# Performance work log

Measured on AMD Instinct MI355X. Metric: run time of the kernel, lower is better.

## Reference

```python
import jax, jax.numpy as jnp
import numpy as np

B, W, F = 32, 128, 64      # batch, window (node feat dim), n_features (nodes)
H, D = 2, 128              # num_heads, out_window_size
NEG_SLOPE = 0.2


def setup_inputs() -> dict:
    key = jax.random.key(0)
    k1, k2, k3, k4, k5 = jax.random.split(key, 5)
    s = 1.0 / np.sqrt(W)
    return {
        "x": jax.random.normal(k1, (B, W, F), dtype=jnp.float32),
        "Wl": jax.random.normal(k2, (W, H * D), dtype=jnp.float32) * s,   # fc_src
        "Wr": jax.random.normal(k3, (W, H * D), dtype=jnp.float32) * s,   # fc_dst
        "attn_a": jax.random.normal(k4, (H, D), dtype=jnp.float32) * s,   # GATv2 attn vector
        "bias": jax.random.normal(k5, (H * D,), dtype=jnp.float32) * 0.01,
    }


def reference(x, Wl, Wr, attn_a, bias):
    """Dense batched GATv2 over a complete graph (with self loops) per batch.

    Matches DGL GATv2Conv (share_weights=False, bias=True, eval mode so
    feat_drop/attn_drop are identity), followed by mean over heads and the
    [B,F,D] -> [B,D,F] transpose of DGLFeatureGAT.forward.
    """
    # node features: x [B, W, F] -> [B, F, W]
    xn = jnp.swapaxes(x, 1, 2)
    el = jnp.einsum('bnw,whd->bnhd', xn, Wl.reshape(W, H, D))  # fc_src(h)
    er = jnp.einsum('bnw,whd->bnhd', xn, Wr.reshape(W, H, D))  # fc_dst(h)
    # edge (src=j -> dst=i): e_ij = a_h . LeakyReLU(el_j + er_i)
    pair = el[:, None, :, :, :] + er[:, :, None, :, :]          # [B, i, j, H, D]
    e = jnp.einsum('bijhd,hd->bhij', jax.nn.leaky_relu(pair, NEG_SLOPE), attn_a)
    # softmax over incoming edges (src j) per dst i
    alpha = jax.nn.softmax(e, axis=-1)                          # [B, H, i, j]
    rst = jnp.einsum('bhij,bjhd->bihd', alpha, el)              # aggregate fc_src feats
    rst = rst + bias.reshape(1, 1, H, D)
    out = rst.mean(axis=2)                                      # mean over heads -> [B, F, D]
    return jnp.swapaxes(out, 1, 2)                              # [B, D, F]
```

## Files before the change

### kernel.cpp

```cpp
#include <hip/hip_runtime.h>
#include <hip/hip_bf16.h>


constexpr int kB = 32, kW = 128, kF = 64, kH = 2, kD = 128, kHD = 256;
constexpr float kNeg = 0.2f;

__device__ __forceinline__ float lrelu(float v) { return fmaxf(v, kNeg * v); }

__global__ __launch_bounds__(512) void gat_proj(
    const float* __restrict__ x, const float* __restrict__ Wl,
    const float* __restrict__ Wr, float* __restrict__ elw,
    float* __restrict__ erw) {
  __shared__ float xw[kW][kF + 4];
  __shared__ float wls[kW][32];
  __shared__ float wrs[kW][32];
  const int b = blockIdx.x >> 3;
  const int c0 = (blockIdx.x & 7) << 5;
  const int t = threadIdx.x;

  const float* xb = x + b * (kW * kF);
#pragma unroll
  for (int k = 0; k < 16; ++k) {
    const int idx = t + (k << 9);
    xw[idx >> 6][idx & 63] = xb[idx];
  }
#pragma unroll
  for (int k = 0; k < 2; ++k) {
    const int s = t + (k << 9);
    const int w = s >> 3;
    const int cc = (s & 7) << 2;
    *(float4*)&wls[w][cc] = *(const float4*)&Wl[w * kHD + c0 + cc];
    *(float4*)&wrs[w][cc] = *(const float4*)&Wr[w * kHD + c0 + cc];
  }
  __syncthreads();

  const int cl = t & 31;
  const int c = c0 + cl;
  const int n0 = (t >> 5) << 2;
  float accl[4] = {0.f, 0.f, 0.f, 0.f};
  float accr[4] = {0.f, 0.f, 0.f, 0.f};

#pragma unroll 4
  for (int w = 0; w < kW; ++w) {
    const float wl = wls[w][cl];
    const float wr = wrs[w][cl];
    const float4 xa = *(const float4*)&xw[w][n0];
    accl[0] = fmaf(xa.x, wl, accl[0]); accr[0] = fmaf(xa.x, wr, accr[0]);
    accl[1] = fmaf(xa.y, wl, accl[1]); accr[1] = fmaf(xa.y, wr, accr[1]);
    accl[2] = fmaf(xa.z, wl, accl[2]); accr[2] = fmaf(xa.z, wr, accr[2]);
    accl[3] = fmaf(xa.w, wl, accl[3]); accr[3] = fmaf(xa.w, wr, accr[3]);
  }

  const int base = (b * kF + n0) * kHD + c;
#pragma unroll
  for (int k = 0; k < 4; ++k) {
    elw[base + k * kHD] = accl[k];
    erw[base + k * kHD] = accr[k];
  }
}

__global__ __launch_bounds__(512) void gat_attn(
    const float* __restrict__ elw, const float* __restrict__ erw,
    const float* __restrict__ attn_a, const float* __restrict__ bias,
    float* __restrict__ out) {
  __shared__ float el[kH][kF][kD + 4];
  __shared__ float er[kH][8][kD + 4];
  __shared__ float av[kH][kD];
  __shared__ float sT[kH][kF][13];

  const int b = blockIdx.x >> 3;
  const int i0 = (blockIdx.x & 7) << 3;
  const int t = threadIdx.x;

  {
    const float* elb = elw + b * (kF * kHD);
#pragma unroll
    for (int k = 0; k < 8; ++k) {
      const int s = t + (k << 9);
      const int h = s >> 11;
      const int n = (s >> 5) & 63;
      const int dv = (s & 31) << 2;
      *(float4*)&el[h][n][dv] = *(const float4*)&elb[n * kHD + h * kD + dv];
    }
    const float* erb = erw + (b * kF + i0) * kHD;
    {
      const int h = t >> 8;
      const int r = (t >> 5) & 7;
      const int dv = (t & 31) << 2;
      *(float4*)&er[h][r][dv] = *(const float4*)&erb[r * kHD + h * kD + dv];
    }
    if (t < kH * kD) av[t >> 7][t & 127] = attn_a[t];
  }
  __syncthreads();

  {
    const int q = t & 15;
    const int i = (t >> 4) & 7;
    const int h = (t >> 7) & 1;
    const int j0 = q + ((t >> 8) << 5);
    const int j1 = j0 + 16;
    float e0 = 0.f, e1 = 0.f;
#pragma unroll
    for (int dv = 0; dv < kD; dv += 4) {
      const float4 rv = *(const float4*)&er[h][i][dv];
      const float4 a4 = *(const float4*)&av[h][dv];
      const float4 p0 = *(const float4*)&el[h][j0][dv];
      const float4 p1 = *(const float4*)&el[h][j1][dv];
      e0 = fmaf(lrelu(p0.x + rv.x), a4.x, e0);
      e0 = fmaf(lrelu(p0.y + rv.y), a4.y, e0);
      e0 = fmaf(lrelu(p0.z + rv.z), a4.z, e0);
      e0 = fmaf(lrelu(p0.w + rv.w), a4.w, e0);
      e1 = fmaf(lrelu(p1.x + rv.x), a4.x, e1);
      e1 = fmaf(lrelu(p1.y + rv.y), a4.y, e1);
      e1 = fmaf(lrelu(p1.z + rv.z), a4.z, e1);
      e1 = fmaf(lrelu(p1.w + rv.w), a4.w, e1);
    }
    sT[h][j0][i] = e0;
    sT[h][j1][i] = e1;
  }
  __syncthreads();

  {
    const int q = t & 31;
    const int g = t >> 5;
    const int i = g & 7;
    const int h = g >> 3;
    const float v0 = sT[h][q][i];
    const float v1 = sT[h][q + 32][i];
    float m = fmaxf(v0, v1);
#pragma unroll
    for (int off = 1; off < 32; off <<= 1) m = fmaxf(m, __shfl_xor(m, off));
    const float x0 = __expf(v0 - m);
    const float x1 = __expf(v1 - m);
    float s = x0 + x1;
#pragma unroll
    for (int off = 1; off < 32; off <<= 1) s += __shfl_xor(s, off);
    const float inv = 1.f / s;
    sT[h][q][i] = x0 * inv;
    sT[h][q + 32][i] = x1 * inv;
  }
  __syncthreads();

  {
    const int i = t & 7;
    const int dh = (t >> 3) << 1;
    float a00 = 0.f, a01 = 0.f, a10 = 0.f, a11 = 0.f;
#pragma unroll 4
    for (int j = 0; j < kF; ++j) {
      const float al0 = sT[0][j][i];
      const float al1 = sT[1][j][i];
      const float2 e0 = *(const float2*)&el[0][j][dh];
      const float2 e1 = *(const float2*)&el[1][j][dh];
      a00 = fmaf(al0, e0.x, a00);
      a01 = fmaf(al0, e0.y, a01);
      a10 = fmaf(al1, e1.x, a10);
      a11 = fmaf(al1, e1.y, a11);
    }
    const float bs0 = bias[dh] + bias[kD + dh];
    const float bs1 = bias[dh + 1] + bias[kD + dh + 1];
    float* ob = out + b * (kD * kF) + i0 + i;
    ob[dh * kF] = 0.5f * (a00 + a10 + bs0);
    ob[(dh + 1) * kF] = 0.5f * (a01 + a11 + bs1);
  }
}

extern "C" void kernel_launch(void* const* d_in, const int* in_sizes, int n_in,
                              void* d_out, int out_size, void* d_ws,
                              size_t ws_size, hipStream_t stream) {
  (void)in_sizes; (void)n_in; (void)ws_size; (void)out_size;
  const float* x = (const float*)d_in[0];
  const float* Wl = (const float*)d_in[1];
  const float* Wr = (const float*)d_in[2];
  const float* attn_a = (const float*)d_in[3];
  const float* bias = (const float*)d_in[4];
  float* out = (float*)d_out;

  float* elw = (float*)d_ws;
  float* erw = elw + (size_t)kB * kF * kHD;

  gat_proj<<<dim3(kB * 8), dim3(512), 0, stream>>>(x, Wl, Wr, elw, erw);
  gat_attn<<<dim3(kB * 8), dim3(512), 0, stream>>>(elw, erw, attn_a, bias, out);
}
```

Baseline: 25.88 us.

## Fuse softmax into score warps and register-tile the aggregation with split-j reduction

The projection kernel now reads Wl/Wr columns straight from global memory instead of staging them in shared memory, and unrolls its loop further. In the attention kernel, thread mapping is changed so each 32-lane warp holds all 64 scores for one (h,i); the softmax then runs on registers, which removes one barrier and the shared round trip. The aggregation uses 4x4 register tiles (4 dst rows x 4 d) over 16-j chunks, writes partials to a new shared buffer and reduces them in a final pass. This adds about 34KB of shared memory, which may lower occupancy.

Result: faster. 24.39 us, median of 3 (-5.8%).

```diff
diff --git a/kernel.cpp b/kernel.cpp
--- a/kernel.cpp
+++ b/kernel.cpp
@@ -12,8 +12,6 @@
     const float* __restrict__ Wr, float* __restrict__ elw,
     float* __restrict__ erw) {
   __shared__ float xw[kW][kF + 4];
-  __shared__ float wls[kW][32];
-  __shared__ float wrs[kW][32];
   const int b = blockIdx.x >> 3;
   const int c0 = (blockIdx.x & 7) << 5;
   const int t = threadIdx.x;
@@ -24,26 +22,19 @@
     const int idx = t + (k << 9);
     xw[idx >> 6][idx & 63] = xb[idx];
   }
-#pragma unroll
-  for (int k = 0; k < 2; ++k) {
-    const int s = t + (k << 9);
-    const int w = s >> 3;
-    const int cc = (s & 7) << 2;
-    *(float4*)&wls[w][cc] = *(const float4*)&Wl[w * kHD + c0 + cc];
-    *(float4*)&wrs[w][cc] = *(const float4*)&Wr[w * kHD + c0 + cc];
-  }
-  __syncthreads();
-
-  const int cl = t & 31;
-  const int c = c0 + cl;
+  __syncthreads();
+
+  const int c = c0 + (t & 31);
   const int n0 = (t >> 5) << 2;
   float accl[4] = {0.f, 0.f, 0.f, 0.f};
   float accr[4] = {0.f, 0.f, 0.f, 0.f};
-
-#pragma unroll 4
+  const float* wlp = Wl + c;
+  const float* wrp = Wr + c;
+
+#pragma unroll 8
   for (int w = 0; w < kW; ++w) {
-    const float wl = wls[w][cl];
-    const float wr = wrs[w][cl];
+    const float wl = wlp[w * kHD];
+    const float wr = wrp[w * kHD];
     const float4 xa = *(const float4*)&xw[w][n0];
     accl[0] = fmaf(xa.x, wl, accl[0]); accr[0] = fmaf(xa.x, wr, accr[0]);
     accl[1] = fmaf(xa.y, wl, accl[1]); accr[1] = fmaf(xa.y, wr, accr[1]);
@@ -66,7 +57,8 @@
   __shared__ float el[kH][kF][kD + 4];
   __shared__ float er[kH][8][kD + 4];
   __shared__ float av[kH][kD];
-  __shared__ float sT[kH][kF][13];
+  __shared__ float sAT[kH][kF][8];
+  __shared__ float pbuf[4][kH][8][kD + 4];
 
   const int b = blockIdx.x >> 3;
   const int i0 = (blockIdx.x & 7) << 3;
@@ -95,9 +87,10 @@
 
   {
     const int q = t & 15;
-    const int i = (t >> 4) & 7;
-    const int h = (t >> 7) & 1;
-    const int j0 = q + ((t >> 8) << 5);
+    const int jh = (t >> 4) & 1;
+    const int i = (t >> 5) & 7;
+    const int h = t >> 8;
+    const int j0 = q + (jh << 5);
     const int j1 = j0 + 16;
     float e0 = 0.f, e1 = 0.f;
 #pragma unroll
@@ -115,52 +108,76 @@
       e1 = fmaf(lrelu(p1.z + rv.z), a4.z, e1);
       e1 = fmaf(lrelu(p1.w + rv.w), a4.w, e1);
     }
-    sT[h][j0][i] = e0;
-    sT[h][j1][i] = e1;
-  }
-  __syncthreads();
-
-  {
-    const int q = t & 31;
-    const int g = t >> 5;
-    const int i = g & 7;
-    const int h = g >> 3;
-    const float v0 = sT[h][q][i];
-    const float v1 = sT[h][q + 32][i];
-    float m = fmaxf(v0, v1);
+    float m = fmaxf(e0, e1);
 #pragma unroll
     for (int off = 1; off < 32; off <<= 1) m = fmaxf(m, __shfl_xor(m, off));
-    const float x0 = __expf(v0 - m);
-    const float x1 = __expf(v1 - m);
+    const float x0 = __expf(e0 - m);
+    const float x1 = __expf(e1 - m);
     float s = x0 + x1;
 #pragma unroll
     for (int off = 1; off < 32; off <<= 1) s += __shfl_xor(s, off);
     const float inv = 1.f / s;
-    sT[h][q][i] = x0 * inv;
-    sT[h][q + 32][i] = x1 * inv;
+    sAT[h][j0][i] = x0 * inv;
+    sAT[h][j1][i] = x1 * inv;
+  }
+  __syncthreads();
+
+  {
+    const int dq = t & 31;
+    const int ip = (t >> 5) & 1;
+    const int jq = (t >> 6) & 3;
+    const int h = t >> 8;
+    float acc[4][4] = {};
+    const int jbase = jq << 4;
+#pragma unroll
+    for (int jj = 0; jj < 16; ++jj) {
+      const int j = jbase + jj;
+      const float4 al = *(const float4*)&sAT[h][j][ip << 2];
+      const float4 ev = *(const float4*)&el[h][j][dq << 2];
+      acc[0][0] = fmaf(al.x, ev.x, acc[0][0]);
+      acc[0][1] = fmaf(al.x, ev.y, acc[0][1]);
+      acc[0][2] = fmaf(al.x, ev.z, acc[0][2]);
+      acc[0][3] = fmaf(al.x, ev.w, acc[0][3]);
+      acc[1][0] = fmaf(al.y, ev.x, acc[1][0]);
+      acc[1][1] = fmaf(al.y, ev.y, acc[1][1]);
+      acc[1][2] = fmaf(al.y, ev.z, acc[1][2]);
+      acc[1][3] = fmaf(al.y, ev.w, acc[1][3]);
+      acc[2][0] = fmaf(al.z, ev.x, acc[2][0]);
+      acc[2][1] = fmaf(al.z, ev.y, acc[2][1]);
+      acc[2][2] = fmaf(al.z, ev.z, acc[2][2]);
+      acc[2][3] = fmaf(al.z, ev.w, acc[2][3]);
+      acc[3][0] = fmaf(al.w, ev.x, acc[3][0]);
+      acc[3][1] = fmaf(al.w, ev.y, acc[3][1]);
+      acc[3][2] = fmaf(al.w, ev.z, acc[3][2]);
+      acc[3][3] = fmaf(al.w, ev.w, acc[3][3]);
+    }
+#pragma unroll
+    for (int ii = 0; ii < 4; ++ii) {
+      float4 v;
+      v.x = acc[ii][0]; v.y = acc[ii][1]; v.z = acc[ii][2]; v.w = acc[ii][3];
+      *(float4*)&pbuf[jq][h][(ip << 2) + ii][dq << 2] = v;
+    }
   }
   __syncthreads();
 
   {
     const int i = t & 7;
-    const int dh = (t >> 3) << 1;
-    float a00 = 0.f, a01 = 0.f, a10 = 0.f, a11 = 0.f;
-#pragma unroll 4
-    for (int j = 0; j < kF; ++j) {
-      const float al0 = sT[0][j][i];
-      const float al1 = sT[1][j][i];
-      const float2 e0 = *(const float2*)&el[0][j][dh];
-      const float2 e1 = *(const float2*)&el[1][j][dh];
-      a00 = fmaf(al0, e0.x, a00);
-      a01 = fmaf(al0, e0.y, a01);
-      a10 = fmaf(al1, e1.x, a10);
-      a11 = fmaf(al1, e1.y, a11);
-    }
-    const float bs0 = bias[dh] + bias[kD + dh];
-    const float bs1 = bias[dh + 1] + bias[kD + dh + 1];
+    const int d = (t >> 3) << 1;
+    float o0 = 0.f, o1 = 0.f;
+#pragma unroll
+    for (int jq = 0; jq < 4; ++jq) {
+#pragma unroll
+      for (int h = 0; h < 2; ++h) {
+        const float2 v = *(const float2*)&pbuf[jq][h][i][d];
+        o0 += v.x;
+        o1 += v.y;
+      }
+    }
+    const float b0 = bias[d] + bias[kD + d];
+    const float b1 = bias[d + 1] + bias[kD + d + 1];
     float* ob = out + b * (kD * kF) + i0 + i;
-    ob[dh * kF] = 0.5f * (a00 + a10 + bs0);
-    ob[(dh + 1) * kF] = 0.5f * (a01 + a11 + bs1);
+    ob[d * kF] = 0.5f * (o0 + b0);
+    ob[(d + 1) * kF] = 0.5f * (o1 + b1);
   }
 }
 
```
